# Kernel optimization log

Measured on AMD Instinct MI355X. Metric: run time of the kernel, lower is better.

## Reference

```python
import jax, jax.numpy as jnp
import numpy as np


def setup_inputs() -> dict:
    key = jax.random.key(0)
    k1, k2, k3 = jax.random.split(key, 3)
    B, S, D_IN, D_OUT = 4, 2048, 4096, 4096
    x = jax.random.normal(k1, (B, S, D_IN), dtype=jnp.float32)
    # int8 quantized weight, stored as int8 (values in [-127, 127])
    weight = jax.random.randint(k2, (D_OUT, D_IN), -127, 128, dtype=jnp.int8)
    weight_scaler = jax.random.uniform(k3, (D_OUT,), dtype=jnp.float32) * 0.02
    return {"x": x, "weight": weight, "weight_scaler": weight_scaler}


def reference(x, weight, weight_scaler):
    # quant path: dequantize weight with per-output-channel scale, then F.linear
    w = weight.astype(jnp.float32) * weight_scaler[:, None]  # [D_OUT, D_IN]
    # F.linear(x, w) == x @ w.T
    return jnp.einsum('bsd,od->bso', x, w)
```

## Files before the change

### kernel.cpp

```cpp
#include <hip/hip_runtime.h>
#include <cstdint>
#include <cstddef>

typedef int i32x4 __attribute__((ext_vector_type(4)));

__global__ __launch_bounds__(256) void prep_kernel(
    const float* __restrict__ x, signed char* __restrict__ xq, float* __restrict__ xs,
    const int* __restrict__ w, signed char* __restrict__ wq,
    int K, int xrows) {
  const int t = threadIdx.x;
  if ((int)blockIdx.x < xrows) {
    const int row = blockIdx.x;
    const float4* xr = (const float4*)(x + (size_t)row * K);
    const int n4 = K >> 2;
    float amax = 0.f;
    for (int i = t; i < n4; i += 256) {
      float4 v = xr[i];
      amax = fmaxf(amax, fmaxf(fmaxf(fabsf(v.x), fabsf(v.y)),
                               fmaxf(fabsf(v.z), fabsf(v.w))));
    }
#pragma unroll
    for (int off = 32; off > 0; off >>= 1)
      amax = fmaxf(amax, __shfl_xor(amax, off, 64));
    __shared__ float wmax[4];
    if ((t & 63) == 0) wmax[t >> 6] = amax;
    __syncthreads();
    amax = fmaxf(fmaxf(wmax[0], wmax[1]), fmaxf(wmax[2], wmax[3]));
    const float inv = (amax > 0.f) ? 127.f / amax : 0.f;
    if (t == 0) xs[row] = amax / 127.f;
    int* o = (int*)(xq + (size_t)row * K);
    for (int i = t; i < n4; i += 256) {
      float4 v = xr[i];
      int a = __float2int_rn(v.x * inv) & 0xFF;
      int b = __float2int_rn(v.y * inv) & 0xFF;
      int c = __float2int_rn(v.z * inv) & 0xFF;
      int d = __float2int_rn(v.w * inv) & 0xFF;
      o[i] = a | (b << 8) | (c << 16) | (d << 24);
    }
  } else {
    const size_t g = (size_t)(blockIdx.x - xrows) * 256 + t;
    int4 v = ((const int4*)w)[g];
    ((int*)wq)[g] = (v.x & 0xFF) | ((v.y & 0xFF) << 8) |
                    ((v.z & 0xFF) << 16) | ((v.w & 0xFF) << 24);
  }
}

static __device__ __forceinline__ void gld_lds16(const void* g, void* l) {
  __builtin_amdgcn_global_load_lds(
      (const __attribute__((address_space(1))) unsigned int*)g,
      (__attribute__((address_space(3))) unsigned int*)l,
      16, 0, 0);
}

__global__ __launch_bounds__(256) void gemm_i8_kernel(
    const signed char* __restrict__ A,
    const signed char* __restrict__ B,
    const float* __restrict__ xs,
    const float* __restrict__ ws,
    float* __restrict__ C,
    int M, int N, int K) {
  __shared__ __align__(16) signed char As[128 * 64];
  __shared__ __align__(16) signed char Bs[128 * 64];

  const int tid  = threadIdx.x;
  const int lane = tid & 63;
  const int wave = tid >> 6;
  const int wm   = wave >> 1;
  const int wn   = wave & 1;
  const int q    = lane >> 4;
  const int r16  = lane & 15;

  const int m0 = blockIdx.y * 128;
  const int n0 = blockIdx.x * 128;

  i32x4 acc[4][4];
#pragma unroll
  for (int i = 0; i < 4; ++i)
#pragma unroll
    for (int j = 0; j < 4; ++j) acc[i][j] = (i32x4){0, 0, 0, 0};

  const int  crow = tid >> 2;
  const int  ccol = (((tid & 3) ^ ((tid >> 3) & 3)) * 16);
  const size_t rs = (size_t)K;
  const char* Ag = (const char*)A + ((size_t)m0 + crow) * rs + ccol;
  const char* Bg = (const char*)B + ((size_t)n0 + crow) * rs + ccol;
  const size_t half = 64 * rs;

  char* AsW = (char*)As + wave * 1024;
  char* BsW = (char*)Bs + wave * 1024;

  const int sw   = (r16 >> 1) & 3;
  const int aoff = (wm * 64 + r16) * 64 + (q ^ sw) * 16;
  const int boff = (wn * 64 + r16) * 64 + (q ^ sw) * 16;

  for (int k0 = 0; k0 < K; k0 += 64) {
    gld_lds16(Ag + k0,        AsW);
    gld_lds16(Ag + k0 + half, AsW + 4096);
    gld_lds16(Bg + k0,        BsW);
    gld_lds16(Bg + k0 + half, BsW + 4096);
    __syncthreads();

    i32x4 af[4], bfr[4];
#pragma unroll
    for (int mt = 0; mt < 4; ++mt)
      af[mt] = *(const i32x4*)(As + aoff + mt * (16 * 64));
#pragma unroll
    for (int nt = 0; nt < 4; ++nt)
      bfr[nt] = *(const i32x4*)(Bs + boff + nt * (16 * 64));
#pragma unroll
    for (int mt = 0; mt < 4; ++mt)
#pragma unroll
      for (int nt = 0; nt < 4; ++nt)
        acc[mt][nt] = __builtin_amdgcn_mfma_i32_16x16x64_i8(
            af[mt], bfr[nt], acc[mt][nt], 0, 0, 0);
    __syncthreads();
  }

  float xsv[4][4];
#pragma unroll
  for (int mt = 0; mt < 4; ++mt) {
    const int row0 = m0 + wm * 64 + mt * 16 + q * 4;
#pragma unroll
    for (int r = 0; r < 4; ++r) xsv[mt][r] = xs[row0 + r];
  }
#pragma unroll
  for (int nt = 0; nt < 4; ++nt) {
    const int col = n0 + wn * 64 + nt * 16 + r16;
    const float s = ws[col];
#pragma unroll
    for (int mt = 0; mt < 4; ++mt) {
      const int row0 = m0 + wm * 64 + mt * 16 + q * 4;
      float* Cp = C + (size_t)row0 * N + col;
#pragma unroll
      for (int r = 0; r < 4; ++r)
        Cp[(size_t)r * N] = (float)acc[mt][nt][r] * xsv[mt][r] * s;
    }
  }
}

__global__ void naive_kernel(const float* __restrict__ x, const int* __restrict__ w,
                             const float* __restrict__ sc, float* __restrict__ out,
                             int M, int N, int K) {
  int idx = blockIdx.x * 256 + threadIdx.x;
  if (idx >= M * N) return;
  int m = idx / N, n = idx % N;
  const float* xr = x + (size_t)m * K;
  const int*   wr = w + (size_t)n * K;
  float acc = 0.f;
  for (int k = 0; k < K; ++k) acc += xr[k] * (float)wr[k];
  out[idx] = acc * sc[n];
}

extern "C" void kernel_launch(void* const* d_in, const int* in_sizes, int n_in,
                              void* d_out, int out_size, void* d_ws, size_t ws_size,
                              hipStream_t stream) {
  const float* x  = (const float*)d_in[0];
  const int*   w  = (const int*)d_in[1];
  const float* sc = (const float*)d_in[2];
  float* out = (float*)d_out;

  const int N = in_sizes[2];
  const int K = in_sizes[1] / N;
  const int M = in_sizes[0] / K;

  const size_t need = (size_t)M * K + (size_t)N * K + (size_t)M * 4 + 16;
  if (ws_size < need || (M % 128) || (N % 128) || (K % 64) || (K % 16) ||
      (((size_t)N * K) % 1024)) {
    int total = M * N;
    naive_kernel<<<(total + 255) / 256, 256, 0, stream>>>(x, w, sc, out, M, N, K);
    return;
  }

  signed char* xq = (signed char*)d_ws;
  signed char* wq = xq + (size_t)M * K;
  float*       xsc = (float*)(wq + (size_t)N * K);

  const int wblocks = (int)(((size_t)N * K) / 1024);
  prep_kernel<<<M + wblocks, 256, 0, stream>>>(x, xq, xsc, w, wq, K, M);

  dim3 grid(N / 128, M / 128);
  gemm_i8_kernel<<<grid, 256, 0, stream>>>(xq, wq, xsc, sc, out, M, N, K);
}
```

Baseline: 461.3 us.

## Rewrite int8 GEMM as 256x256 tile with multi-stage LDS pipelined phases

The int8 MFMA GEMM now uses 256x256 block tiles with 8 waves, K-steps of 128 and a 128KB double-buffered LDS. Each K-step is split into four phases that issue async global-to-LDS loads for later stages while MFMAs run, with explicit waitcnt, barriers and setprio. This is meant to hide global load latency and raise arithmetic intensity compared with the old single-buffered 128x128 loop. The cost is heavy LDS use (one block per CU), a larger register footprint, and stricter shape requirements on the fast path.

```diff
diff --git a/kernel.cpp b/kernel.cpp
--- a/kernel.cpp
+++ b/kernel.cpp
@@ -52,88 +52,119 @@
       16, 0, 0);
 }
 
-__global__ __launch_bounds__(256) void gemm_i8_kernel(
+__global__ __launch_bounds__(512, 2) void gemm_i8_8ph(
     const signed char* __restrict__ A,
     const signed char* __restrict__ B,
     const float* __restrict__ xs,
     const float* __restrict__ ws,
     float* __restrict__ C,
     int M, int N, int K) {
-  __shared__ __align__(16) signed char As[128 * 64];
-  __shared__ __align__(16) signed char Bs[128 * 64];
+  __shared__ __align__(16) signed char lds[131072];
 
   const int tid  = threadIdx.x;
   const int lane = tid & 63;
   const int wave = tid >> 6;
-  const int wm   = wave >> 1;
-  const int wn   = wave & 1;
+  const int wm   = wave >> 2;
+  const int wn   = wave & 3;
   const int q    = lane >> 4;
   const int r16  = lane & 15;
-
-  const int m0 = blockIdx.y * 128;
-  const int n0 = blockIdx.x * 128;
-
-  i32x4 acc[4][4];
-#pragma unroll
-  for (int i = 0; i < 4; ++i)
+  const int e    = lane & 7;
+
+  const int m0 = blockIdx.y << 8;
+  const int n0 = blockIdx.x << 8;
+  const int NT  = K >> 7;
+  const int NT4 = NT << 2;
+
+  const int srow   = tid >> 3;
+  const int schunk = ((tid & 7) ^ (srow & 7)) << 4;
+  const signed char* sA = A + (size_t)(m0 + srow) * K + schunk;
+  const signed char* sB = B + (size_t)(n0 + srow) * K + schunk;
+  signed char* lW = lds + wave * 1024;
+
+  const int aro = ((wm << 4) + r16) << 7;
+  const int bro = r16 << 7;
+  const int cs  = (q ^ e) << 4;
+
+  i32x4 acc[8][4];
+#pragma unroll
+  for (int i = 0; i < 8; ++i)
 #pragma unroll
     for (int j = 0; j < 4; ++j) acc[i][j] = (i32x4){0, 0, 0, 0};
-
-  const int  crow = tid >> 2;
-  const int  ccol = (((tid & 3) ^ ((tid >> 3) & 3)) * 16);
-  const size_t rs = (size_t)K;
-  const char* Ag = (const char*)A + ((size_t)m0 + crow) * rs + ccol;
-  const char* Bg = (const char*)B + ((size_t)n0 + crow) * rs + ccol;
-  const size_t half = 64 * rs;
-
-  char* AsW = (char*)As + wave * 1024;
-  char* BsW = (char*)Bs + wave * 1024;
-
-  const int sw   = (r16 >> 1) & 3;
-  const int aoff = (wm * 64 + r16) * 64 + (q ^ sw) * 16;
-  const int boff = (wn * 64 + r16) * 64 + (q ^ sw) * 16;
-
-  for (int k0 = 0; k0 < K; k0 += 64) {
-    gld_lds16(Ag + k0,        AsW);
-    gld_lds16(Ag + k0 + half, AsW + 4096);
-    gld_lds16(Bg + k0,        BsW);
-    gld_lds16(Bg + k0 + half, BsW + 4096);
-    __syncthreads();
-
-    i32x4 af[4], bfr[4];
-#pragma unroll
-    for (int mt = 0; mt < 4; ++mt)
-      af[mt] = *(const i32x4*)(As + aoff + mt * (16 * 64));
-#pragma unroll
-    for (int nt = 0; nt < 4; ++nt)
-      bfr[nt] = *(const i32x4*)(Bs + boff + nt * (16 * 64));
-#pragma unroll
-    for (int mt = 0; mt < 4; ++mt)
-#pragma unroll
-      for (int nt = 0; nt < 4; ++nt)
-        acc[mt][nt] = __builtin_amdgcn_mfma_i32_16x16x64_i8(
-            af[mt], bfr[nt], acc[mt][nt], 0, 0, 0);
-    __syncthreads();
-  }
-
-  float xsv[4][4];
-#pragma unroll
-  for (int mt = 0; mt < 4; ++mt) {
-    const int row0 = m0 + wm * 64 + mt * 16 + q * 4;
-#pragma unroll
-    for (int r = 0; r < 4; ++r) xsv[mt][r] = xs[row0 + r];
-  }
-#pragma unroll
-  for (int nt = 0; nt < 4; ++nt) {
-    const int col = n0 + wn * 64 + nt * 16 + r16;
-    const float s = ws[col];
-#pragma unroll
-    for (int mt = 0; mt < 4; ++mt) {
-      const int row0 = m0 + wm * 64 + mt * 16 + q * 4;
+  i32x4 af[4][2], bf[2][2];
+
+#define STAGE(Gv)                                                            \
+  do {                                                                       \
+    const int G_ = (Gv);                                                     \
+    if (G_ < NT4) {                                                          \
+      const int t_ = G_ >> 2;                                                \
+      const int half_ = (G_ >> 1) & 1;                                       \
+      signed char* l_ = lW + ((t_ & 1) << 15) + ((G_ & 1) << 16) +           \
+                        (half_ << 14);                                       \
+      const signed char* g_ = ((G_ & 1) ? sB : sA) +                         \
+                              (size_t)(half_ << 7) * K + ((size_t)t_ << 7);  \
+      gld_lds16(g_, l_);                                                     \
+      gld_lds16(g_ + (size_t)64 * K, l_ + 8192);                             \
+    }                                                                        \
+  } while (0)
+
+#define PHASE(MH, NH, READA, Gv, VMW)                                        \
+  do {                                                                       \
+    if (READA) {                                                             \
+      _Pragma("unroll") for (int i_ = 0; i_ < 4; ++i_)                       \
+        _Pragma("unroll") for (int kh_ = 0; kh_ < 2; ++kh_)                  \
+          af[i_][kh_] = *(const i32x4*)(pA + ((((MH) << 2) + i_) << 12) +    \
+                                        aro + (cs ^ (kh_ << 6)));            \
+    }                                                                        \
+    _Pragma("unroll") for (int j_ = 0; j_ < 2; ++j_)                         \
+      _Pragma("unroll") for (int kh_ = 0; kh_ < 2; ++kh_)                    \
+        bf[j_][kh_] = *(const i32x4*)(pB + ((NH) << 14) + (wn << 12) +       \
+                                      (j_ << 11) + bro + (cs ^ (kh_ << 6))); \
+    STAGE(Gv);                                                               \
+    __builtin_amdgcn_s_barrier();                                            \
+    asm volatile("s_waitcnt lgkmcnt(0)" ::: "memory");                       \
+    __builtin_amdgcn_s_setprio(1);                                           \
+    _Pragma("unroll") for (int kh_ = 0; kh_ < 2; ++kh_)                      \
+      _Pragma("unroll") for (int i_ = 0; i_ < 4; ++i_)                       \
+        _Pragma("unroll") for (int j_ = 0; j_ < 2; ++j_)                     \
+          acc[((MH) << 2) + i_][((NH) << 1) + j_] =                          \
+              __builtin_amdgcn_mfma_i32_16x16x64_i8(                         \
+                  af[i_][kh_], bf[j_][kh_],                                  \
+                  acc[((MH) << 2) + i_][((NH) << 1) + j_], 0, 0, 0);         \
+    __builtin_amdgcn_s_setprio(0);                                           \
+    if (VMW) asm volatile("s_waitcnt vmcnt(4)" ::: "memory");                \
+    __builtin_amdgcn_s_barrier();                                            \
+  } while (0)
+
+  STAGE(0); STAGE(1); STAGE(2); STAGE(3); STAGE(4); STAGE(5);
+  asm volatile("s_waitcnt vmcnt(4)" ::: "memory");
+  __builtin_amdgcn_s_barrier();
+
+  for (int t = 0; t < NT; ++t) {
+    const signed char* pA = lds + ((t & 1) << 15);
+    const signed char* pB = lds + 65536 + ((t & 1) << 15);
+    const int G0 = t << 2;
+    PHASE(0, 0, 1, G0 + 6, 0);
+    PHASE(0, 1, 0, G0 + 7, 0);
+    PHASE(1, 0, 1, G0 + 8, 0);
+    PHASE(1, 1, 0, G0 + 9, 1);
+  }
+#undef PHASE
+#undef STAGE
+
+#pragma unroll
+  for (int mt = 0; mt < 8; ++mt) {
+    const int row0 = m0 + (mt << 5) + (wm << 4) + (q << 2);
+    float xv[4];
+#pragma unroll
+    for (int r = 0; r < 4; ++r) xv[r] = xs[row0 + r];
+#pragma unroll
+    for (int nt = 0; nt < 4; ++nt) {
+      const int col = n0 + ((nt >> 1) << 7) + (wn << 5) + ((nt & 1) << 4) + r16;
+      const float s = ws[col];
       float* Cp = C + (size_t)row0 * N + col;
 #pragma unroll
       for (int r = 0; r < 4; ++r)
-        Cp[(size_t)r * N] = (float)acc[mt][nt][r] * xsv[mt][r] * s;
+        Cp[(size_t)r * N] = (float)acc[mt][nt][r] * xv[r] * s;
     }
   }
 }
@@ -164,7 +195,7 @@
   const int M = in_sizes[0] / K;
 
   const size_t need = (size_t)M * K + (size_t)N * K + (size_t)M * 4 + 16;
-  if (ws_size < need || (M % 128) || (N % 128) || (K % 64) || (K % 16) ||
+  if (ws_size < need || (M & 255) || (N & 255) || (K & 127) || K < 256 ||
       (((size_t)N * K) % 1024)) {
     int total = M * N;
     naive_kernel<<<(total + 255) / 256, 256, 0, stream>>>(x, w, sc, out, M, N, K);
@@ -178,6 +209,6 @@
   const int wblocks = (int)(((size_t)N * K) / 1024);
   prep_kernel<<<M + wblocks, 256, 0, stream>>>(x, xq, xsc, w, wq, K, M);
 
-  dim3 grid(N / 128, M / 128);
-  gemm_i8_kernel<<<grid, 256, 0, stream>>>(xq, wq, xsc, sc, out, M, N, K);
-}
+  dim3 grid(N >> 8, M >> 8);
+  gemm_i8_8ph<<<grid, 512, 0, stream>>>(xq, wq, xsc, sc, out, M, N, K);
+}
```

Result: faster. 389.8 us (-15.5%).
